# Performance work log

Hardware: AMD Instinct MI355X
Metric: run time of the kernel (lower is better)

## Reference

```python
import jax, jax.numpy as jnp
import numpy as np

HEADS = 8
DIM = 512
DIM_HEAD = DIM // 8          # 64
LANDMARKS = DIM // 2         # 256
PINV_ITERS = 6
KERNEL = 33                  # residual_conv_kernel default
SCALE = DIM_HEAD ** -0.5


def setup_inputs() -> dict:
    key = jax.random.key(0)
    k0, k1, k2, k3 = jax.random.split(key, 4)
    b, n = 2, 8192
    x = jax.random.normal(k0, (b, n, DIM), dtype=jnp.float32)
    inner = HEADS * DIM_HEAD
    w_qkv = jax.random.normal(k1, (DIM, 3 * inner), dtype=jnp.float32) * 0.02
    w_out = jax.random.normal(k2, (inner, DIM), dtype=jnp.float32) * 0.02
    b_out = jnp.zeros((DIM,), dtype=jnp.float32)
    # grouped depthwise-over-heads conv: (out_ch=H, in_ch/groups=1, kH=33, kW=1)
    w_conv = jax.random.normal(k3, (HEADS, 1, KERNEL, 1), dtype=jnp.float32) * 0.02
    return {"x": x, "w_qkv": w_qkv, "w_out": w_out, "b_out": b_out, "w_conv": w_conv}


def _moore_penrose_pinv(x, iters=PINV_ITERS):
    # x: [b, h, m, m]
    abs_x = jnp.abs(x)
    col = abs_x.sum(axis=-1).max()   # global max over col sums (matches torch.max)
    row = abs_x.sum(axis=-2).max()
    z = jnp.swapaxes(x, -1, -2) / (col * row)
    I = jnp.eye(x.shape[-1], dtype=x.dtype)
    for _ in range(iters):
        xz = x @ z
        z = 0.25 * z @ (13.0 * I - xz @ (15.0 * I - xz @ (7.0 * I - xz)))
    return z


def reference(x, w_qkv, w_out, b_out, w_conv):
    b, n, _ = x.shape
    m = LANDMARKS
    l = n // m  # n chosen divisible by m, so no left-padding branch

    qkv = x @ w_qkv                                   # [b, n, 3*inner]
    q, k, v = jnp.split(qkv, 3, axis=-1)
    to_heads = lambda t: t.reshape(b, n, HEADS, DIM_HEAD).transpose(0, 2, 1, 3)
    q = to_heads(q) * SCALE                           # [b, h, n, d]
    k = to_heads(k)
    v = to_heads(v)

    # landmarks: mean over consecutive groups of l tokens -> [b, h, m, d]
    q_l = q.reshape(b, HEADS, m, l, DIM_HEAD).mean(axis=3)
    k_l = k.reshape(b, HEADS, m, l, DIM_HEAD).mean(axis=3)

    sim1 = jnp.einsum('bhid,bhjd->bhij', q, k_l)      # [b, h, n, m]
    sim2 = jnp.einsum('bhid,bhjd->bhij', q_l, k_l)    # [b, h, m, m]
    sim3 = jnp.einsum('bhid,bhjd->bhij', q_l, k)      # [b, h, m, n]

    attn1 = jax.nn.softmax(sim1, axis=-1)
    attn2 = jax.nn.softmax(sim2, axis=-1)
    attn3 = jax.nn.softmax(sim3, axis=-1)

    attn2_inv = _moore_penrose_pinv(attn2)
    out = attn1 @ (attn2_inv @ (attn3 @ v))           # [b, h, n, d]

    # residual depthwise conv over the sequence dim, per head (groups = heads)
    pad = KERNEL // 2
    res = jax.lax.conv_general_dilated(
        v, w_conv, window_strides=(1, 1), padding=((pad, pad), (0, 0)),
        dimension_numbers=('NCHW', 'OIHW', 'NCHW'), feature_group_count=HEADS)
    out = out + res

    out = out.transpose(0, 2, 1, 3).reshape(b, n, HEADS * DIM_HEAD)
    out = out @ w_out + b_out                         # to_out (dropout = eval no-op)
    return x + out                                    # NyAttenLayer residual
```

## Files before the change

### kernel.cpp

```cpp
#include <hip/hip_runtime.h>
#include <hip/hip_bf16.h>

#define BH 16
#define NTOK 8192
#define NHEAD 8
#define DH 64
#define MLM 256
#define QSCALE 0.125f
#define LP 72
#define LOG2E 1.4426950408889634f

typedef unsigned short ushort_t;
using frag_ab = __attribute__((ext_vector_type(8))) short;
using frag_cd = __attribute__((ext_vector_type(4))) float;

__device__ __forceinline__ unsigned short f2bs(float f){
  __hip_bfloat16 h = __float2bfloat16(f);
  return *(unsigned short*)&h;
}
__device__ __forceinline__ float bs2f(unsigned short u){
  union { unsigned int i; float f; } cv; cv.i = ((unsigned int)u) << 16; return cv.f;
}

__device__ __forceinline__ void gl_lds16(const unsigned short* g, unsigned short* l){
  __builtin_amdgcn_global_load_lds((const __attribute__((address_space(1))) unsigned int*)(const void*)g,
                                   (__attribute__((address_space(3))) unsigned int*)(void*)l, 16, 0, 0);
}

__global__ __launch_bounds__(256) void k_splitw(const float* __restrict__ in, int K, int N,
                                                unsigned short* __restrict__ oh,
                                                unsigned short* __restrict__ ol, int swz){
  const int idx = blockIdx.x * 256 + threadIdx.x;
  const int n = idx / K, k = idx - n * K;
  const float v = in[(size_t)k * N + n];
  const unsigned short hi = f2bs(v);
  int kd = k;
  if (swz){
    const int q = (k >> 3) & 3;
    kd = (k & ~31) | (((q ^ (n & 3)) & 3) << 3) | (k & 7);
  }
  oh[(size_t)n * K + kd] = hi;
  ol[(size_t)n * K + kd] = f2bs(v - bs2f(hi));
}

__global__ __launch_bounds__(256) void k_splitx(const float* __restrict__ in,
                                                unsigned short* __restrict__ oh,
                                                unsigned short* __restrict__ ol){
  const size_t i4 = ((size_t)blockIdx.x * 256 + threadIdx.x) * 4;
  const int row = (int)(i4 >> 9);
  const int col = (int)(i4 & 511);
  const int q = (col >> 3) & 3;
  const int cd = (col & ~31) | (((q ^ (row & 3)) & 3) << 3) | (col & 7);
  const size_t o4 = ((size_t)row << 9) + cd;
  float4 v = *(const float4*)(in + i4);
  const unsigned short h0 = f2bs(v.x), h1 = f2bs(v.y), h2 = f2bs(v.z), h3 = f2bs(v.w);
  *(ushort4*)(oh + o4) = make_ushort4(h0, h1, h2, h3);
  *(ushort4*)(ol + o4) = make_ushort4(f2bs(v.x - bs2f(h0)), f2bs(v.y - bs2f(h1)),
                                      f2bs(v.z - bs2f(h2)), f2bs(v.w - bs2f(h3)));
}

__global__ __launch_bounds__(256) void k_mfma_qkv(const unsigned short* __restrict__ xh,
                                                  const unsigned short* __restrict__ xl,
                                                  const unsigned short* __restrict__ bth,
                                                  const unsigned short* __restrict__ btl,
                                                  float* __restrict__ q,
                                                  unsigned short* __restrict__ kSh,
                                                  unsigned short* __restrict__ kSl,
                                                  float* __restrict__ v){
  const int n0 = blockIdx.x * 128;
  const int m0 = blockIdx.y * 128;
  __shared__ unsigned short Ah[128*32], Al[128*32], Bh[128*32], Bl[128*32];
  const int tid = threadIdx.x;
  const int wave = tid >> 6, lane = tid & 63;
  const int wm = wave >> 1, wn = wave & 1;
  const int lr = lane & 15, quad = lane >> 4;
  const int cswz = ((quad ^ (lr & 3)) & 3) << 3;
  const unsigned short* gsrc = (wave == 0) ? xh : (wave == 1) ? xl : (wave == 2) ? bth : btl;
  unsigned short* lbase = (wave == 0) ? Ah : (wave == 1) ? Al : (wave == 2) ? Bh : Bl;
  const int R0 = (wave < 2) ? m0 : n0;
  const int lrow = lane >> 2, lslot = (lane & 3) << 3;
  frag_cd acc[4][4];
#pragma unroll
  for (int mt = 0; mt < 4; mt++)
#pragma unroll
    for (int nt = 0; nt < 4; nt++){
      frag_cd z = {0.f, 0.f, 0.f, 0.f};
      acc[mt][nt] = z;
    }
  for (int k0 = 0; k0 < 512; k0 += 32){
    __syncthreads();
#pragma unroll
    for (int u = 0; u < 8; u++){
      gl_lds16(gsrc + (size_t)(R0 + u*16 + lrow) * 512 + k0 + lslot, lbase + u * 512);
    }
    __syncthreads();
    frag_ab a_h[4], a_l[4], b_h[4], b_l[4];
#pragma unroll
    for (int t = 0; t < 4; t++){
      const int ar = (wm*64 + t*16 + lr) << 5;
      const int br = (wn*64 + t*16 + lr) << 5;
      a_h[t] = *(const frag_ab*)&Ah[ar + cswz];
      a_l[t] = *(const frag_ab*)&Al[ar + cswz];
      b_h[t] = *(const frag_ab*)&Bh[br + cswz];
      b_l[t] = *(const frag_ab*)&Bl[br + cswz];
    }
#pragma unroll
    for (int mt = 0; mt < 4; mt++)
#pragma unroll
      for (int nt = 0; nt < 4; nt++){
        acc[mt][nt] = __builtin_amdgcn_mfma_f32_16x16x32_bf16(a_l[mt], b_h[nt], acc[mt][nt], 0, 0, 0);
        acc[mt][nt] = __builtin_amdgcn_mfma_f32_16x16x32_bf16(a_h[mt], b_l[nt], acc[mt][nt], 0, 0, 0);
        acc[mt][nt] = __builtin_amdgcn_mfma_f32_16x16x32_bf16(a_h[mt], b_h[nt], acc[mt][nt], 0, 0, 0);
      }
  }
#pragma unroll
  for (int mt = 0; mt < 4; mt++)
#pragma unroll
    for (int nt = 0; nt < 4; nt++)
#pragma unroll
      for (int rg = 0; rg < 4; rg++){
        const int row = m0 + wm*64 + mt*16 + quad*4 + rg;
        const int col = n0 + wn*64 + nt*16 + lr;
        const int bb = row >> 13, i = row & 8191;
        const int which = col >> 9;
        const int cc = col & 511;
        const int h = cc >> 6, d = cc & 63;
        const size_t off = (((size_t)(bb * NHEAD + h)) * NTOK + i) * DH + d;
        const float val = acc[mt][nt][rg];
        if (which == 0)      q[off] = val * QSCALE;
        else if (which == 1){
          const unsigned short hi = f2bs(val);
          kSh[off] = hi; kSl[off] = f2bs(val - bs2f(hi));
        }
        else                 v[off] = val;
      }
}

__global__ __launch_bounds__(256) void k_mfma_final(const unsigned int* __restrict__ qpk,
                                                    const unsigned short* __restrict__ bth,
                                                    const unsigned short* __restrict__ btl,
                                                    const float* __restrict__ xin,
                                                    const float* __restrict__ bout,
                                                    float* __restrict__ outp){
  const int n0 = blockIdx.x * 128;
  const int m0 = blockIdx.y * 128;
  __shared__ unsigned short Ah[128][40], Al[128][40], Bh[128][40], Bl[128][40];
  const int tid = threadIdx.x;
  const int wave = tid >> 6, lane = tid & 63;
  const int wm = wave >> 1, wn = wave & 1;
  const int lr = lane & 15, quad = lane >> 4, koff = quad * 8;
  const int bb = m0 >> 13;
  frag_cd acc[4][4];
#pragma unroll
  for (int mt = 0; mt < 4; mt++)
#pragma unroll
    for (int nt = 0; nt < 4; nt++){
      frag_cd z = {0.f, 0.f, 0.f, 0.f};
      acc[mt][nt] = z;
    }
  for (int k0 = 0; k0 < 512; k0 += 32){
    const int h = k0 >> 6, dbase = k0 & 63;
    __syncthreads();
#pragma unroll
    for (int u = 0; u < 4; u++){
      const int f = tid + u * 256, row = f >> 3, c4 = (f & 7) << 2;
      const int i = (m0 + row) & 8191;
      uint4 pw = *(const uint4*)(qpk + (((size_t)(bb * NHEAD + h)) * NTOK + i) * DH + dbase + c4);
      *(ushort4*)&Ah[row][c4] = make_ushort4((unsigned short)pw.x, (unsigned short)pw.y,
                                             (unsigned short)pw.z, (unsigned short)pw.w);
      *(ushort4*)&Al[row][c4] = make_ushort4((unsigned short)(pw.x >> 16), (unsigned short)(pw.y >> 16),
                                             (unsigned short)(pw.z >> 16), (unsigned short)(pw.w >> 16));
    }
#pragma unroll
    for (int u = 0; u < 2; u++){
      const int f = tid + u * 256, row = f >> 2, ch = (f & 3) << 3;
      *(uint4*)&Bh[row][ch] = *(const uint4*)(bth + (size_t)(n0 + row) * 512 + k0 + ch);
      *(uint4*)&Bl[row][ch] = *(const uint4*)(btl + (size_t)(n0 + row) * 512 + k0 + ch);
    }
    __syncthreads();
    frag_ab a_h[4], a_l[4], b_h[4], b_l[4];
#pragma unroll
    for (int t = 0; t < 4; t++){
      a_h[t] = *(const frag_ab*)&Ah[wm*64 + t*16 + lr][koff];
      a_l[t] = *(const frag_ab*)&Al[wm*64 + t*16 + lr][koff];
      b_h[t] = *(const frag_ab*)&Bh[wn*64 + t*16 + lr][koff];
      b_l[t] = *(const frag_ab*)&Bl[wn*64 + t*16 + lr][koff];
    }
#pragma unroll
    for (int mt = 0; mt < 4; mt++)
#pragma unroll
      for (int nt = 0; nt < 4; nt++){
        acc[mt][nt] = __builtin_amdgcn_mfma_f32_16x16x32_bf16(a_l[mt], b_h[nt], acc[mt][nt], 0, 0, 0);
        acc[mt][nt] = __builtin_amdgcn_mfma_f32_16x16x32_bf16(a_h[mt], b_l[nt], acc[mt][nt], 0, 0, 0);
        acc[mt][nt] = __builtin_amdgcn_mfma_f32_16x16x32_bf16(a_h[mt], b_h[nt], acc[mt][nt], 0, 0, 0);
      }
  }
#pragma unroll
  for (int mt = 0; mt < 4; mt++)
#pragma unroll
    for (int nt = 0; nt < 4; nt++)
#pragma unroll
      for (int rg = 0; rg < 4; rg++){
        const int row = m0 + wm*64 + mt*16 + quad*4 + rg;
        const int col = n0 + wn*64 + nt*16 + lr;
        outp[(size_t)row * 512 + col] = acc[mt][nt][rg] + bout[col] + xin[(size_t)row * 512 + col];
      }
}

__global__ __launch_bounds__(64) void k_land2(const float* __restrict__ qf,
                                              const unsigned short* __restrict__ kSh,
                                              const unsigned short* __restrict__ kSl,
                                              float* __restrict__ qlf, float* __restrict__ klf,
                                              unsigned short* __restrict__ qlSh, unsigned short* __restrict__ qlSl,
                                              unsigned short* __restrict__ klSh, unsigned short* __restrict__ klSl){
  const int isK = blockIdx.y;
  float* dst = isK ? klf : qlf;
  unsigned short* dh = isK ? klSh : qlSh;
  unsigned short* dl = isK ? klSl : qlSl;
  const int bh = blockIdx.x >> 8;
  const int j  = blockIdx.x & 255;
  const int d  = threadIdx.x;
  const size_t base = ((size_t)bh * NTOK + (size_t)j * 32) * DH + d;
  float s = 0.f;
  if (!isK){
    const float* p = qf + base;
#pragma unroll
    for (int t = 0; t < 32; t++) s += p[t * DH];
  } else {
    const unsigned short* ph = kSh + base;
    const unsigned short* pl = kSl + base;
#pragma unroll
    for (int t = 0; t < 32; t++) s += bs2f(ph[t * DH]) + bs2f(pl[t * DH]);
  }
  const float val = s * (1.f / 32.f);
  const size_t oidx = ((size_t)bh * MLM + j) * DH + d;
  dst[oidx] = val;
  const unsigned short hi = f2bs(val);
  dh[oidx] = hi;
  dl[oidx] = f2bs(val - bs2f(hi));
}

__global__ __launch_bounds__(256) void k_vtrans(const float* __restrict__ vf,
                                                unsigned short* __restrict__ vTh,
                                                unsigned short* __restrict__ vTl){
  __shared__ float T[64][68];
  const int j0 = blockIdx.x * 64, bh = blockIdx.y;
  const int tid = threadIdx.x;
#pragma unroll
  for (int u = 0; u < 4; u++){
    const int f = tid + u * 256, row = f >> 4, c4 = (f & 15) << 2;
    *(float4*)&T[row][c4] = *(const float4*)(vf + ((size_t)bh * NTOK + j0 + row) * DH + c4);
  }
  __syncthreads();
#pragma unroll
  for (int u = 0; u < 4; u++){
    const int f = tid + u * 256, d = f >> 4, j4 = (f & 15) << 2;
    const float v0 = T[j4+0][d], v1 = T[j4+1][d], v2 = T[j4+2][d], v3 = T[j4+3][d];
    const unsigned short h0 = f2bs(v0), h1 = f2bs(v1), h2 = f2bs(v2), h3 = f2bs(v3);
    const size_t off = ((size_t)bh * DH + d) * NTOK + j0 + j4;
    *(ushort4*)(vTh + off) = make_ushort4(h0, h1, h2, h3);
    *(ushort4*)(vTl + off) = make_ushort4(f2bs(v0 - bs2f(h0)), f2bs(v1 - bs2f(h1)),
                                          f2bs(v2 - bs2f(h2)), f2bs(v3 - bs2f(h3)));
  }
}

__global__ __launch_bounds__(256) void k_sim2(const float* __restrict__ qlf,
                                              const float* __restrict__ klf,
                                              float* __restrict__ C){
  const int bh = blockIdx.z;
  const float* Ab = qlf + (size_t)bh * MLM * DH;
  const float* Bb = klf + (size_t)bh * MLM * DH;
  float* Cb = C + (size_t)bh * MLM * MLM;
  const int n0 = blockIdx.x * 64;
  const int m0 = blockIdx.y * 64;
  __shared__ float As[16][64];
  __shared__ float Bs[16][64];
  const int tid = threadIdx.x, ty = tid >> 4, tx = tid & 15;
  const int lm = tid >> 2, lk = (tid & 3) << 2;
  float acc[4][4] = {};
  for (int k0 = 0; k0 < 64; k0 += 16){
    float4 a4 = *(const float4*)(Ab + (size_t)(m0 + lm) * DH + k0 + lk);
    As[lk+0][lm] = a4.x; As[lk+1][lm] = a4.y; As[lk+2][lm] = a4.z; As[lk+3][lm] = a4.w;
    float4 b4 = *(const float4*)(Bb + (size_t)(n0 + lm) * DH + k0 + lk);
    Bs[lk+0][lm] = b4.x; Bs[lk+1][lm] = b4.y; Bs[lk+2][lm] = b4.z; Bs[lk+3][lm] = b4.w;
    __syncthreads();
#pragma unroll
    for (int kk = 0; kk < 16; kk++){
      float a[4], bv[4];
#pragma unroll
      for (int r = 0; r < 4; r++) a[r] = As[kk][ty*4 + r];
#pragma unroll
      for (int c = 0; c < 4; c++) bv[c] = Bs[kk][tx*4 + c];
#pragma unroll
      for (int r = 0; r < 4; r++)
#pragma unroll
        for (int c = 0; c < 4; c++) acc[r][c] += a[r] * bv[c];
    }
    __syncthreads();
  }
#pragma unroll
  for (int r = 0; r < 4; r++)
#pragma unroll
    for (int c = 0; c < 4; c++)
      Cb[(size_t)(m0 + ty*4 + r) * MLM + n0 + tx*4 + c] = acc[r][c];
}

__global__ __launch_bounds__(256) void k_softmax256(const float* __restrict__ in, float* __restrict__ outp){
  const int row = blockIdx.x;
  const int t = threadIdx.x;
  float v = in[(size_t)row * 256 + t];
  __shared__ float red[256];
  red[t] = v; __syncthreads();
  for (int o = 128; o > 0; o >>= 1){ if (t < o) red[t] = fmaxf(red[t], red[t+o]); __syncthreads(); }
  float mx = red[0]; __syncthreads();
  float e = exp2f((v - mx) * LOG2E);
  red[t] = e; __syncthreads();
  for (int o = 128; o > 0; o >>= 1){ if (t < o) red[t] += red[t+o]; __syncthreads(); }
  outp[(size_t)row * 256 + t] = e / red[0];
}

__global__ __launch_bounds__(256) void k_colrow(const float* __restrict__ a2, float* __restrict__ part){
  const int bh = blockIdx.x;
  const int t = threadIdx.x;
  const float* p = a2 + (size_t)bh * 65536;
  float cs = 0.f;
  for (int i = 0; i < 256; i++) cs += fabsf(p[(size_t)i * 256 + t]);
  __shared__ float r2[256];
  r2[t] = cs; __syncthreads();
  for (int o = 128; o > 0; o >>= 1){
    if (t < o) r2[t] = fmaxf(r2[t], r2[t+o]);
    __syncthreads();
  }
  if (t == 0) part[bh] = r2[0];
}

__global__ __launch_bounds__(256) void k_z0(const float* __restrict__ a2, const float* __restrict__ part,
                                            float* __restrict__ z,
                                            unsigned short* __restrict__ zTh,
                                            unsigned short* __restrict__ zTl){
  const int bh = blockIdx.x >> 8;
  const int i  = blockIdx.x & 255;
  const int j  = threadIdx.x;
  float m2 = 0.f;
#pragma unroll
  for (int t = 0; t < 16; t++) m2 = fmaxf(m2, part[t]);
  const float sc = 1.f / m2;
  const size_t ridx = ((size_t)bh * 256 + j) * 256 + i;
  const float val = a2[ridx] * sc;
  z[((size_t)bh * 256 + i) * 256 + j] = val;
  const unsigned short hi = f2bs(val);
  zTh[ridx] = hi;
  zTl[ridx] = f2bs(val - bs2f(hi));
}

__global__ __launch_bounds__(256) void k_gemm256m(const float* __restrict__ A,
                                                  const unsigned short* __restrict__ BTh,
                                                  const unsigned short* __restrict__ BTl,
                                                  const float* __restrict__ D,
                                                  float* __restrict__ C,
                                                  unsigned short* __restrict__ CTh,
                                                  unsigned short* __restrict__ CTl,
                                                  float c0, float s0, int wC){
  __shared__ unsigned short Ah[32][40], Al[32][40], Bh[64][40], Bl[64][40];
  __shared__ float Ct[64][33];
  const int bh = blockIdx.y, tile = blockIdx.x;
  const int m0 = (tile >> 2) * 32, n0 = (tile & 3) * 64;
  const size_t bo = (size_t)bh * 65536;
  const int tid = threadIdx.x;
  const int wave = tid >> 6, lane = tid & 63;
  const int wm = wave >> 1, wn = wave & 1;
  const int lr = lane & 15, quad = lane >> 4, koff = quad * 8;
  const int ar = tid >> 3, ac = (tid & 7) << 2;
  const int br = tid >> 2, bc = (tid & 3) << 3;
  frag_cd acc[2];
  { frag_cd z = {0.f,0.f,0.f,0.f}; acc[0] = z; acc[1] = z; }
  float4 ra  = *(const float4*)(A + bo + (size_t)(m0 + ar) * 256 + ac);
  uint4  rbh = *(const uint4*)(BTh + bo + (size_t)(n0 + br) * 256 + bc);
  uint4  rbl = *(const uint4*)(BTl + bo + (size_t)(n0 + br) * 256 + bc);
  for (int k0 = 0; k0 < 256; k0 += 32){
    __syncthreads();
    {
      const unsigned short h0=f2bs(ra.x),h1=f2bs(ra.y),h2=f2bs(ra.z),h3=f2bs(ra.w);
      *(ushort4*)&Ah[ar][ac] = make_ushort4(h0,h1,h2,h3);
      *(ushort4*)&Al[ar][ac] = make_ushort4(f2bs(ra.x-bs2f(h0)), f2bs(ra.y-bs2f(h1)),
                                            f2bs(ra.z-bs2f(h2)), f2bs(ra.w-bs2f(h3)));
      *(uint4*)&Bh[br][bc] = rbh;
      *(uint4*)&Bl[br][bc] = rbl;
    }
    __syncthreads();
    if (k0 < 224){
      ra  = *(const float4*)(A + bo + (size_t)(m0 + ar) * 256 + k0 + 32 + ac);
      rbh = *(const uint4*)(BTh + bo + (size_t)(n0 + br) * 256 + k0 + 32 + bc);
      rbl = *(const uint4*)(BTl + bo + (size_t)(n0 + br) * 256 + k0 + 32 + bc);
    }
    frag_ab a_h = *(const frag_ab*)&Ah[wm*16 + lr][koff];
    frag_ab a_l = *(const frag_ab*)&Al[wm*16 + lr][koff];
#pragma unroll
    for (int b = 0; b < 2; b++){
      frag_ab b_h = *(const frag_ab*)&Bh[wn*32 + b*16 + lr][koff];
      frag_ab b_l = *(const frag_ab*)&Bl[wn*32 + b*16 + lr][koff];
      acc[b] = __builtin_amdgcn_mfma_f32_16x16x32_bf16(a_l, b_l, acc[b], 0, 0, 0);
      acc[b] = __builtin_amdgcn_mfma_f32_16x16x32_bf16(a_l, b_h, acc[b], 0, 0, 0);
      acc[b] = __builtin_amdgcn_mfma_f32_16x16x32_bf16(a_h, b_l, acc[b], 0, 0, 0);
      acc[b] = __builtin_amdgcn_mfma_f32_16x16x32_bf16(a_h, b_h, acc[b], 0, 0, 0);
    }
  }
  const bool useD = (c0 != 0.f);
#pragma unroll
  for (int b = 0; b < 2; b++)
#pragma unroll
    for (int rg = 0; rg < 4; rg++){
      const int row = m0 + wm*16 + quad*4 + rg;
      const int col = n0 + wn*32 + b*16 + lr;
      const size_t idx = bo + (size_t)row * 256 + col;
      const float dv = useD ? D[idx] : 0.f;
      const float val = s0 * (c0 * dv - acc[b][rg]);
      if (wC) C[idx] = val;
      Ct[col - n0][row - m0] = val;
    }
  __syncthreads();
  {
    const int cr = tid >> 2, sg = (tid & 3) << 3;
    unsigned int ph[4], pl[4];
#pragma unroll
    for (int j = 0; j < 4; j++){
      const float v0 = Ct[cr][sg + 2*j], v1 = Ct[cr][sg + 2*j + 1];
      const unsigned short h0 = f2bs(v0), h1 = f2bs(v1);
      ph[j] = (unsigned int)h0 | ((unsigned int)h1 << 16);
      pl[j] = (unsigned int)f2bs(v0 - bs2f(h0)) | ((unsigned int)f2bs(v1 - bs2f(h1)) << 16);
    }
    const size_t tb = bo + (size_t)(n0 + cr) * 256 + m0 + sg;
    *(uint4*)(CTh + tb) = make_uint4(ph[0], ph[1], ph[2], ph[3]);
    *(uint4*)(CTl + tb) = make_uint4(pl[0], pl[1], pl[2], pl[3]);
  }
}

__global__ __launch_bounds__(256) void k_flash(const unsigned short* __restrict__ qlSh,
                                               const unsigned short* __restrict__ qlSl,
                                               const unsigned short* __restrict__ kSh,
                                               const unsigned short* __restrict__ kSl,
                                               const unsigned short* __restrict__ vTh,
                                               const unsigned short* __restrict__ vTl,
                                               float* __restrict__ pbuf){
  extern __shared__ __align__(16) unsigned short sm[];
  unsigned short* Kh  = sm;
  unsigned short* Kl  = sm + 1*64*LP;
  unsigned short* Wth = sm + 2*64*LP;
  unsigned short* Wtl = sm + 3*64*LP;
  const int kc = blockIdx.x, mt = blockIdx.y, bh = blockIdx.z;
  const int m0 = mt * 64, kbeg = kc * 512;
  const int tid = threadIdx.x;
  const int wave = tid >> 6, lane = tid & 63;
  const int lr = lane & 15, quad = lane >> 4;
  const size_t qbase = (size_t)bh * MLM * DH;
  const size_t kb  = (size_t)bh * NTOK * DH;
  const size_t vtb = (size_t)bh * DH * NTOK;
#pragma unroll
  for (int u = 0; u < 4; u++){
    const int f = tid + u * 256, row = f >> 4, c4 = (f & 15) << 2;
    *(ushort4*)&Kh[row*LP + c4] = *(const ushort4*)(qlSh + qbase + (size_t)(m0 + row) * DH + c4);
    *(ushort4*)&Kl[row*LP + c4] = *(const ushort4*)(qlSl + qbase + (size_t)(m0 + row) * DH + c4);
  }
  __syncthreads();
  frag_ab qa_h[2], qa_l[2];
#pragma unroll
  for (int ks = 0; ks < 2; ks++){
    const int ao = (wave*16 + lr)*LP + ks*32 + quad*8;
    qa_h[ks] = *(const frag_ab*)&Kh[ao];
    qa_l[ks] = *(const frag_ab*)&Kl[ao];
  }
  float m_run[4], l_run[4];
  frag_cd o[4];
#pragma unroll
  for (int r = 0; r < 4; r++){ m_run[r] = -1e30f; l_run[r] = 0.f; }
#pragma unroll
  for (int nt = 0; nt < 4; nt++){ frag_cd z = {0.f,0.f,0.f,0.f}; o[nt] = z; }

  for (int ch = 0; ch < 8; ch++){
    const int kr0 = kbeg + ch * 64;
    __syncthreads();
#pragma unroll
    for (int u = 0; u < 4; u++){
      const int f = tid + u * 256, row = f >> 4, c4 = (f & 15) << 2;
      *(ushort4*)&Kh[row*LP + c4]  = *(const ushort4*)(kSh + kb + (size_t)(kr0 + row) * DH + c4);
      *(ushort4*)&Kl[row*LP + c4]  = *(const ushort4*)(kSl + kb + (size_t)(kr0 + row) * DH + c4);
      *(ushort4*)&Wth[row*LP + c4] = *(const ushort4*)(vTh + vtb + (size_t)row * NTOK + kr0 + c4);
      *(ushort4*)&Wtl[row*LP + c4] = *(const ushort4*)(vTl + vtb + (size_t)row * NTOK + kr0 + c4);
    }
    __syncthreads();
    frag_cd s[4];
#pragma unroll
    for (int nt = 0; nt < 4; nt++){ frag_cd z = {0.f,0.f,0.f,0.f}; s[nt] = z; }
#pragma unroll
    for (int ks = 0; ks < 2; ks++){
#pragma unroll
      for (int nt = 0; nt < 4; nt++){
        const int bo = (nt*16 + lr)*LP + ks*32 + quad*8;
        frag_ab b_h = *(const frag_ab*)&Kh[bo];
        frag_ab b_l = *(const frag_ab*)&Kl[bo];
        s[nt] = __builtin_amdgcn_mfma_f32_16x16x32_bf16(qa_l[ks], b_h, s[nt], 0, 0, 0);
        s[nt] = __builtin_amdgcn_mfma_f32_16x16x32_bf16(qa_h[ks], b_l, s[nt], 0, 0, 0);
        s[nt] = __builtin_amdgcn_mfma_f32_16x16x32_bf16(qa_h[ks], b_h, s[nt], 0, 0, 0);
      }
    }
    __syncthreads();
#pragma unroll
    for (int rg = 0; rg < 4; rg++){
      float mx = fmaxf(fmaxf(s[0][rg], s[1][rg]), fmaxf(s[2][rg], s[3][rg]));
#pragma unroll
      for (int o2 = 8; o2 >= 1; o2 >>= 1) mx = fmaxf(mx, __shfl_xor(mx, o2));
      const float mnew = fmaxf(m_run[rg], mx);
      float e0 = exp2f((s[0][rg] - mnew) * LOG2E), e1 = exp2f((s[1][rg] - mnew) * LOG2E);
      float e2 = exp2f((s[2][rg] - mnew) * LOG2E), e3 = exp2f((s[3][rg] - mnew) * LOG2E);
      float psum = e0 + e1 + e2 + e3;
#pragma unroll
      for (int o2 = 8; o2 >= 1; o2 >>= 1) psum += __shfl_xor(psum, o2);
      const float alpha = exp2f((m_run[rg] - mnew) * LOG2E);
      l_run[rg] = l_run[rg] * alpha + psum;
      m_run[rg] = mnew;
#pragma unroll
      for (int nt = 0; nt < 4; nt++) o[nt][rg] *= alpha;
      const int prow = (wave*16 + quad*4 + rg) * LP;
      float ee[4] = {e0, e1, e2, e3};
#pragma unroll
      for (int nt = 0; nt < 4; nt++){
        const unsigned short hh = f2bs(ee[nt]);
        Kh[prow + nt*16 + lr] = hh;
        Kl[prow + nt*16 + lr] = f2bs(ee[nt] - bs2f(hh));
      }
    }
#pragma unroll
    for (int ks = 0; ks < 2; ks++){
      const int ao = (wave*16 + lr)*LP + ks*32 + quad*8;
      frag_ab p_h = *(const frag_ab*)&Kh[ao];
      frag_ab p_l = *(const frag_ab*)&Kl[ao];
#pragma unroll
      for (int nt = 0; nt < 4; nt++){
        const int bo = (nt*16 + lr)*LP + ks*32 + quad*8;
        frag_ab b_h = *(const frag_ab*)&Wth[bo];
        frag_ab b_l = *(const frag_ab*)&Wtl[bo];
        o[nt] = __builtin_amdgcn_mfma_f32_16x16x32_bf16(p_l, b_h, o[nt], 0, 0, 0);
        o[nt] = __builtin_amdgcn_mfma_f32_16x16x32_bf16(p_h, b_l, o[nt], 0, 0, 0);
        o[nt] = __builtin_amdgcn_mfma_f32_16x16x32_bf16(p_h, b_h, o[nt], 0, 0, 0);
      }
    }
  }
  float* pb = pbuf + (((size_t)bh * 16 + kc) * 256 + m0) * 68;
#pragma unroll
  for (int rg = 0; rg < 4; rg++){
    const int row = wave*16 + quad*4 + rg;
#pragma unroll
    for (int nt = 0; nt < 4; nt++)
      pb[(size_t)row * 68 + nt*16 + lr] = o[nt][rg];
    if (lr == 0){
      pb[(size_t)row * 68 + 64] = m_run[rg];
      pb[(size_t)row * 68 + 65] = l_run[rg];
    }
  }
}

__global__ __launch_bounds__(256) void k_comb(const float* __restrict__ pbuf, float* __restrict__ av){
  const int wv = threadIdx.x >> 6, lane = threadIdx.x & 63;
  const int id = blockIdx.x * 4 + wv;
  const int bh = id >> 8, row = id & 255;
  const float* base = pbuf + ((size_t)bh * 16 * 256 + row) * 68;
  float M = -1e30f;
#pragma unroll
  for (int k = 0; k < 16; k++) M = fmaxf(M, base[(size_t)k * 256 * 68 + 64]);
  float L = 0.f, o = 0.f;
#pragma unroll
  for (int k = 0; k < 16; k++){
    const float* p = base + (size_t)k * 256 * 68;
    float w = exp2f((p[64] - M) * LOG2E);
    L += p[65] * w;
    o += p[lane] * w;
  }
  av[((size_t)bh * MLM + row) * DH + lane] = o / L;
}

__global__ __launch_bounds__(256) void k_w2(const float* __restrict__ Z, const float* __restrict__ AV,
                                            float* __restrict__ W2,
                                            unsigned short* __restrict__ w2Th,
                                            unsigned short* __restrict__ w2Tl){
  const int bh = blockIdx.y, mt = blockIdx.x;
  const float* Zb = Z + (size_t)bh * 65536;
  const float* Vb = AV + (size_t)bh * MLM * DH;
  float* Wb = W2 + (size_t)bh * MLM * DH;
  const int m0 = mt * 64;
  __shared__ float As[16][64];
  __shared__ float Bs[16][64];
  const int tid = threadIdx.x, ty = tid >> 4, tx = tid & 15;
  const int lm = tid >> 2, lk = (tid & 3) << 2;
  const int lk2 = tid >> 4, ln = (tid & 15) << 2;
  float acc[4][4] = {};
  for (int k0 = 0; k0 < 256; k0 += 16){
    float4 a4 = *(const float4*)(Zb + (size_t)(m0 + lm) * 256 + k0 + lk);
    As[lk+0][lm] = a4.x; As[lk+1][lm] = a4.y; As[lk+2][lm] = a4.z; As[lk+3][lm] = a4.w;
    float4 b4 = *(const float4*)(Vb + (size_t)(k0 + lk2) * DH + ln);
    *(float4*)&Bs[lk2][ln] = b4;
    __syncthreads();
#pragma unroll
    for (int kk = 0; kk < 16; kk++){
      float a[4], bv[4];
#pragma unroll
      for (int r = 0; r < 4; r++) a[r] = As[kk][ty*4 + r];
#pragma unroll
      for (int c = 0; c < 4; c++) bv[c] = Bs[kk][tx*4 + c];
#pragma unroll
      for (int r = 0; r < 4; r++)
#pragma unroll
        for (int c = 0; c < 4; c++) acc[r][c] += a[r] * bv[c];
    }
    __syncthreads();
  }
#pragma unroll
  for (int r = 0; r < 4; r++)
#pragma unroll
    for (int c = 0; c < 4; c++){
      const float val = acc[r][c];
      Wb[(size_t)(m0 + ty*4 + r) * DH + tx*4 + c] = val;
      const unsigned short hi = f2bs(val);
      const size_t tidx = ((size_t)bh * DH + tx*4 + c) * MLM + m0 + ty*4 + r;
      w2Th[tidx] = hi;
      w2Tl[tidx] = f2bs(val - bs2f(hi));
    }
}

__global__ __launch_bounds__(512) void k_attn1(float* __restrict__ qoh,
                                               const unsigned short* __restrict__ klSh,
                                               const unsigned short* __restrict__ klSl,
                                               const float* __restrict__ vf,
                                               const unsigned short* __restrict__ w2Th,
                                               const unsigned short* __restrict__ w2Tl,
                                               const float* __restrict__ wconv){
  extern __shared__ __align__(16) unsigned short sm[];
  unsigned short* Kh  = sm;
  unsigned short* Kl  = sm + 1*64*LP;
  unsigned short* Wth = sm + 2*64*LP;
  unsigned short* Wtl = sm + 3*64*LP;
  unsigned short* Ph  = sm + 4*64*LP;
  unsigned short* Pl  = sm + 6*64*LP;
  float (*Vs)[68] = (float (*)[68])sm;
  float (*St)[68] = (float (*)[68])sm;
  __shared__ float wcs[33];
  const int it = blockIdx.x, bh = blockIdx.y, h = bh & 7;
  const int i0 = it * 128;
  float* qb = qoh + (size_t)bh * NTOK * DH;
  const int tid = threadIdx.x;
  const int wave = tid >> 6, lane = tid & 63;
  const int lr = lane & 15, quad = lane >> 4;
  if (tid < 33) wcs[tid] = wconv[h*33 + tid];
  frag_ab qa_h[2], qa_l[2];
#pragma unroll
  for (int ks = 0; ks < 2; ks++){
    const float* qsrc = qb + (size_t)(i0 + wave*16 + lr) * DH + ks*32 + quad*8;
    float4 a0 = *(const float4*)qsrc;
    float4 a1 = *(const float4*)(qsrc + 4);
    float vv[8] = {a0.x, a0.y, a0.z, a0.w, a1.x, a1.y, a1.z, a1.w};
    frag_ab fh, fl;
#pragma unroll
    for (int j = 0; j < 8; j++){
      const unsigned short hb = f2bs(vv[j]);
      fh[j] = (short)hb;
      fl[j] = (short)f2bs(vv[j] - bs2f(hb));
    }
    qa_h[ks] = fh; qa_l[ks] = fl;
  }
  float m_run[4], l_run[4];
  frag_cd o[4];
#pragma unroll
  for (int r = 0; r < 4; r++){ m_run[r] = -1e30f; l_run[r] = 0.f; }
#pragma unroll
  for (int nt = 0; nt < 4; nt++){ frag_cd z = {0.f,0.f,0.f,0.f}; o[nt] = z; }
  const size_t klbase = (size_t)bh * MLM * DH;
  const size_t wtbase = (size_t)bh * DH * MLM;

  for (int jc = 0; jc < 4; jc++){
    const int j0 = jc * 64;
    __syncthreads();
#pragma unroll
    for (int u = 0; u < 2; u++){
      const int f = tid + u * 512, row = f >> 4, c4 = (f & 15) << 2;
      *(ushort4*)&Kh[row*LP + c4]  = *(const ushort4*)(klSh + klbase + (size_t)(j0 + row) * DH + c4);
      *(ushort4*)&Kl[row*LP + c4]  = *(const ushort4*)(klSl + klbase + (size_t)(j0 + row) * DH + c4);
      *(ushort4*)&Wth[row*LP + c4] = *(const ushort4*)(w2Th + wtbase + (size_t)row * MLM + j0 + c4);
      *(ushort4*)&Wtl[row*LP + c4] = *(const ushort4*)(w2Tl + wtbase + (size_t)row * MLM + j0 + c4);
    }
    __syncthreads();
    frag_cd s[4];
#pragma unroll
    for (int nt = 0; nt < 4; nt++){ frag_cd z = {0.f,0.f,0.f,0.f}; s[nt] = z; }
#pragma unroll
    for (int ks = 0; ks < 2; ks++){
#pragma unroll
      for (int nt = 0; nt < 4; nt++){
        const int bo = (nt*16 + lr)*LP + ks*32 + quad*8;
        frag_ab b_h = *(const frag_ab*)&Kh[bo];
        frag_ab b_l = *(const frag_ab*)&Kl[bo];
        s[nt] = __builtin_amdgcn_mfma_f32_16x16x32_bf16(qa_l[ks], b_h, s[nt], 0, 0, 0);
        s[nt] = __builtin_amdgcn_mfma_f32_16x16x32_bf16(qa_h[ks], b_l, s[nt], 0, 0, 0);
        s[nt] = __builtin_amdgcn_mfma_f32_16x16x32_bf16(qa_h[ks], b_h, s[nt], 0, 0, 0);
      }
    }
#pragma unroll
    for (int rg = 0; rg < 4; rg++){
      float mx = fmaxf(fmaxf(s[0][rg], s[1][rg]), fmaxf(s[2][rg], s[3][rg]));
#pragma unroll
      for (int o2 = 8; o2 >= 1; o2 >>= 1) mx = fmaxf(mx, __shfl_xor(mx, o2));
      const float mnew = fmaxf(m_run[rg], mx);
      float e0 = exp2f((s[0][rg] - mnew) * LOG2E), e1 = exp2f((s[1][rg] - mnew) * LOG2E);
      float e2 = exp2f((s[2][rg] - mnew) * LOG2E), e3 = exp2f((s[3][rg] - mnew) * LOG2E);
      float psum = e0 + e1 + e2 + e3;
#pragma unroll
      for (int o2 = 8; o2 >= 1; o2 >>= 1) psum += __shfl_xor(psum, o2);
      const float alpha = exp2f((m_run[rg] - mnew) * LOG2E);
      l_run[rg] = l_run[rg] * alpha + psum;
      m_run[rg] = mnew;
#pragma unroll
      for (int nt = 0; nt < 4; nt++) o[nt][rg] *= alpha;
      const int prow = (wave*16 + quad*4 + rg) * LP;
      float ee[4] = {e0, e1, e2, e3};
#pragma unroll
      for (int nt = 0; nt < 4; nt++){
        const unsigned short hh = f2bs(ee[nt]);
        Ph[prow + nt*16 + lr] = hh;
        Pl[prow + nt*16 + lr] = f2bs(ee[nt] - bs2f(hh));
      }
    }
#pragma unroll
    for (int ks = 0; ks < 2; ks++){
      const int ao = (wave*16 + lr)*LP + ks*32 + quad*8;
      frag_ab p_h = *(const frag_ab*)&Ph[ao];
      frag_ab p_l = *(const frag_ab*)&Pl[ao];
#pragma unroll
      for (int nt = 0; nt < 4; nt++){
        const int bo = (nt*16 + lr)*LP + ks*32 + quad*8;
        frag_ab b_h = *(const frag_ab*)&Wth[bo];
        frag_ab b_l = *(const frag_ab*)&Wtl[bo];
        o[nt] = __builtin_amdgcn_mfma_f32_16x16x32_bf16(p_l, b_h, o[nt], 0, 0, 0);
        o[nt] = __builtin_amdgcn_mfma_f32_16x16x32_bf16(p_h, b_l, o[nt], 0, 0, 0);
        o[nt] = __builtin_amdgcn_mfma_f32_16x16x32_bf16(p_h, b_h, o[nt], 0, 0, 0);
      }
    }
  }
#pragma unroll
  for (int rg = 0; rg < 4; rg++){
    const float inv = 1.f / l_run[rg];
#pragma unroll
    for (int nt = 0; nt < 4; nt++) o[nt][rg] *= inv;
  }
  __syncthreads();
#pragma unroll
  for (int u = 0; u < 5; u++){
    const int f = tid + u * 512, row = f >> 4, c4 = (f & 15) << 2;
    const int g = i0 - 16 + row;
    float4 vv = make_float4(0.f, 0.f, 0.f, 0.f);
    if (g >= 0 && g < NTOK) vv = *(const float4*)(vf + ((size_t)bh * NTOK + g) * DH + c4);
    *(float4*)&Vs[row][c4] = vv;
  }
  __syncthreads();
  const int rbase = wave*16 + quad*4;
#pragma unroll
  for (int nt = 0; nt < 4; nt++){
    const int col = nt*16 + lr;
#pragma unroll
    for (int s5 = 0; s5 < 36; s5++){
      const float v = Vs[rbase + s5][col];
#pragma unroll
      for (int rg = 0; rg < 4; rg++){
        const int t = s5 - rg;
        if (t >= 0 && t <= 32) o[nt][rg] += wcs[t] * v;
      }
    }
  }
  __syncthreads();
#pragma unroll
  for (int nt = 0; nt < 4; nt++)
#pragma unroll
    for (int rg = 0; rg < 4; rg++){
      const float val = o[nt][rg];
      const unsigned short hi = f2bs(val);
      const unsigned short lo = f2bs(val - bs2f(hi));
      St[rbase + rg][nt*16 + lr] = __uint_as_float((unsigned int)hi | ((unsigned int)lo << 16));
    }
  __syncthreads();
#pragma unroll
  for (int u = 0; u < 4; u++){
    const int f = tid + u * 512, row = f >> 4, c4 = (f & 15) << 2;
    *(float4*)(qb + (size_t)(i0 + row) * DH + c4) = *(const float4*)&St[row][c4];
  }
}

extern "C" void kernel_launch(void* const* d_in, const int* in_sizes, int n_in,
                              void* d_out, int out_size, void* d_ws, size_t ws_size,
                              hipStream_t stream){
  (void)in_sizes; (void)n_in; (void)out_size; (void)ws_size;
  const float* x     = (const float*)d_in[0];
  const float* wqkv  = (const float*)d_in[1];
  const float* wout  = (const float*)d_in[2];
  const float* bout  = (const float*)d_in[3];
  const float* wconv = (const float*)d_in[4];
  float* outp = (float*)d_out;

  char* base = (char*)d_ws;
  auto alloc = [&](size_t bytes)->char*{
    char* p = base; base += (bytes + 255) & ~(size_t)255; return p;
  };
  const size_t QS = (size_t)BH * NTOK * DH;
  const size_t LS = (size_t)BH * MLM * DH;
  const size_t MM = (size_t)BH * MLM * MLM;

  float* qf   = (float*)alloc(QS * 4);
  float* vf   = (float*)alloc(QS * 4);
  unsigned short* kSh = (unsigned short*)alloc(QS * 2);
  unsigned short* kSl = (unsigned short*)alloc(QS * 2);
  float* qlf  = (float*)alloc(LS * 4);
  float* klf  = (float*)alloc(LS * 4);
  float* a2   = (float*)alloc(MM * 4);
  float* zb   = (float*)alloc(MM * 4);
  float* z2   = (float*)alloc(MM * 4);
  float* xz   = (float*)alloc(MM * 4);
  float* t2   = (float*)alloc(MM * 4);
  float* t4   = (float*)alloc(MM * 4);
  float* part = (float*)alloc(64 * 4);
  char* un = alloc(10 * MM * 2);
  unsigned short* pl0 = (unsigned short*)un;
  unsigned short* zbTh = pl0 + 0*MM; unsigned short* zbTl = pl0 + 1*MM;
  unsigned short* z2Th = pl0 + 2*MM; unsigned short* z2Tl = pl0 + 3*MM;
  unsigned short* xzTh = pl0 + 4*MM; unsigned short* xzTl = pl0 + 5*MM;
  unsigned short* t2Th = pl0 + 6*MM; unsigned short* t2Tl = pl0 + 7*MM;
  unsigned short* t4Th = pl0 + 8*MM; unsigned short* t4Tl = pl0 + 9*MM;
  float* pbuf = (float*)un;
  float* av   = (float*)alloc(LS * 4);
  float* w2   = (float*)alloc(LS * 4);
  unsigned short* wqTh = (unsigned short*)alloc((size_t)1536 * 512 * 2);
  unsigned short* wqTl = (unsigned short*)alloc((size_t)1536 * 512 * 2);
  unsigned short* woTh = (unsigned short*)alloc((size_t)512 * 512 * 2);
  unsigned short* woTl = (unsigned short*)alloc((size_t)512 * 512 * 2);
  unsigned short* qlSh = (unsigned short*)alloc(LS * 2);
  unsigned short* qlSl = (unsigned short*)alloc(LS * 2);
  unsigned short* klSh = (unsigned short*)alloc(LS * 2);
  unsigned short* klSl = (unsigned short*)alloc(LS * 2);
  unsigned short* w2Th = (unsigned short*)alloc(LS * 2);
  unsigned short* w2Tl = (unsigned short*)alloc(LS * 2);
  unsigned short* vTh  = (unsigned short*)alloc(QS * 2);
  unsigned short* vTl  = (unsigned short*)alloc(QS * 2);
  unsigned short* xh = vTh;
  unsigned short* xl = vTl;

  k_splitw<<<1536 * 512 / 256, 256, 0, stream>>>(wqkv, 512, 1536, wqTh, wqTl, 1);
  k_splitw<<<512 * 512 / 256, 256, 0, stream>>>(wout, 512, 512, woTh, woTl, 0);
  k_splitx<<<8192, 256, 0, stream>>>(x, xh, xl);
  k_mfma_qkv<<<dim3(12, 128), 256, 0, stream>>>(xh, xl, wqTh, wqTl, qf, kSh, kSl, vf);
  k_vtrans<<<dim3(NTOK / 64, BH), 256, 0, stream>>>(vf, vTh, vTl);
  k_land2<<<dim3(BH * MLM, 2), 64, 0, stream>>>(qf, kSh, kSl, qlf, klf, qlSh, qlSl, klSh, klSl);
  k_sim2<<<dim3(4, 4, BH), 256, 0, stream>>>(qlf, klf, xz);
  k_softmax256<<<BH * MLM, 256, 0, stream>>>(xz, a2);
  k_colrow<<<BH, 256, 0, stream>>>(a2, part);
  k_z0<<<BH * MLM, 256, 0, stream>>>(a2, part, zb, zbTh, zbTl);
  {
    float* zc = zb;  unsigned short* zcTh = zbTh; unsigned short* zcTl = zbTl;
    float* zn = z2;  unsigned short* znTh = z2Th; unsigned short* znTl = z2Tl;
    for (int it = 0; it < 6; ++it){
      k_gemm256m<<<dim3(32, BH), 256, 0, stream>>>(a2, zcTh, zcTl, a2, xz, xzTh, xzTl, 0.f, -1.f, 1);
      k_gemm256m<<<dim3(32, BH), 256, 0, stream>>>(xz, xzTh, xzTl, xz, t2, t2Th, t2Tl, 7.f, 1.f, 0);
      k_gemm256m<<<dim3(32, BH), 256, 0, stream>>>(xz, t2Th, t2Tl, xz, t4, t4Th, t4Tl, 15.f, 1.f, 0);
      k_gemm256m<<<dim3(32, BH), 256, 0, stream>>>(zc, t4Th, t4Tl, zc, zn, znTh, znTl, 13.f, 0.25f, 1);
      float* tf = zc; zc = zn; zn = tf;
      unsigned short* th = zcTh; zcTh = znTh; znTh = th;
      unsigned short* tl = zcTl; zcTl = znTl; znTl = tl;
    }
  }
  const size_t FLASH_LDS = (size_t)4 * 64 * LP * 2;
  const size_t ATTN1_LDS = (size_t)8 * 64 * LP * 2;
  k_flash<<<dim3(16, 4, BH), 256, FLASH_LDS, stream>>>(qlSh, qlSl, kSh, kSl, vTh, vTl, pbuf);
  k_comb<<<BH * MLM / 4, 256, 0, stream>>>(pbuf, av);
  k_w2<<<dim3(4, BH), 256, 0, stream>>>(zb, av, w2, w2Th, w2Tl);
  k_attn1<<<dim3(64, BH), 512, ATTN1_LDS, stream>>>(qf, klSh, klSl, vf, w2Th, w2Tl, wconv);
  k_mfma_final<<<dim3(4, 128), 256, 0, stream>>>((const unsigned int*)qf, woTh, woTl, x, bout, outp);
}
```

Before: 695.9 us.

## Double-buffer QKV GEMM LDS, prefetch out-proj A tile, drop lo*lo MFMA

The QKV projection GEMM now uses two LDS buffers. The next K-slice is loaded asynchronously into the alternate buffer while MFMAs run on the current one, which cuts one barrier per iteration. The output-projection GEMM prefetches the next packed Q/attention tile into registers before the compute step, so global latency is hidden behind the MFMAs. The pinv GEMM drops the low×low bf16 split-product term, reducing its MFMA work by a quarter at a small accuracy cost in the Newton–Schulz iterations. Double buffering doubles the QKV kernel's LDS use (64KB), which may reduce occupancy.

```diff
diff --git a/kernel.cpp b/kernel.cpp
--- a/kernel.cpp
+++ b/kernel.cpp
@@ -69,16 +69,16 @@
                                                   float* __restrict__ v){
   const int n0 = blockIdx.x * 128;
   const int m0 = blockIdx.y * 128;
-  __shared__ unsigned short Ah[128*32], Al[128*32], Bh[128*32], Bl[128*32];
+  __shared__ unsigned short SB[2][4 * 128 * 32];
   const int tid = threadIdx.x;
   const int wave = tid >> 6, lane = tid & 63;
   const int wm = wave >> 1, wn = wave & 1;
   const int lr = lane & 15, quad = lane >> 4;
   const int cswz = ((quad ^ (lr & 3)) & 3) << 3;
   const unsigned short* gsrc = (wave == 0) ? xh : (wave == 1) ? xl : (wave == 2) ? bth : btl;
-  unsigned short* lbase = (wave == 0) ? Ah : (wave == 1) ? Al : (wave == 2) ? Bh : Bl;
   const int R0 = (wave < 2) ? m0 : n0;
   const int lrow = lane >> 2, lslot = (lane & 3) << 3;
+  const int pbase = wave * 4096;
   frag_cd acc[4][4];
 #pragma unroll
   for (int mt = 0; mt < 4; mt++)
@@ -87,13 +87,22 @@
       frag_cd z = {0.f, 0.f, 0.f, 0.f};
       acc[mt][nt] = z;
     }
+#pragma unroll
+  for (int u = 0; u < 8; u++)
+    gl_lds16(gsrc + (size_t)(R0 + u*16 + lrow) * 512 + lslot, &SB[0][pbase] + u * 512);
+  __syncthreads();
+  int cur = 0;
   for (int k0 = 0; k0 < 512; k0 += 32){
-    __syncthreads();
-#pragma unroll
-    for (int u = 0; u < 8; u++){
-      gl_lds16(gsrc + (size_t)(R0 + u*16 + lrow) * 512 + k0 + lslot, lbase + u * 512);
-    }
-    __syncthreads();
+    if (k0 + 32 < 512){
+#pragma unroll
+      for (int u = 0; u < 8; u++)
+        gl_lds16(gsrc + (size_t)(R0 + u*16 + lrow) * 512 + k0 + 32 + lslot,
+                 &SB[cur ^ 1][pbase] + u * 512);
+    }
+    const unsigned short* Ah = &SB[cur][0];
+    const unsigned short* Al = &SB[cur][4096];
+    const unsigned short* Bh = &SB[cur][8192];
+    const unsigned short* Bl = &SB[cur][12288];
     frag_ab a_h[4], a_l[4], b_h[4], b_l[4];
 #pragma unroll
     for (int t = 0; t < 4; t++){
@@ -112,6 +121,8 @@
         acc[mt][nt] = __builtin_amdgcn_mfma_f32_16x16x32_bf16(a_h[mt], b_l[nt], acc[mt][nt], 0, 0, 0);
         acc[mt][nt] = __builtin_amdgcn_mfma_f32_16x16x32_bf16(a_h[mt], b_h[nt], acc[mt][nt], 0, 0, 0);
       }
+    __syncthreads();
+    cur ^= 1;
   }
 #pragma unroll
   for (int mt = 0; mt < 4; mt++)
@@ -158,26 +169,41 @@
       frag_cd z = {0.f, 0.f, 0.f, 0.f};
       acc[mt][nt] = z;
     }
+  const int arow = tid >> 3, ac4 = (tid & 7) << 2;
+  const int brow = tid >> 2, bch = (tid & 3) << 3;
+  uint4 pw[4];
+#pragma unroll
+  for (int u = 0; u < 4; u++){
+    const int row = arow + u * 32;
+    const int i = (m0 + row) & 8191;
+    pw[u] = *(const uint4*)(qpk + (((size_t)(bb * NHEAD + 0)) * NTOK + i) * DH + 0 + ac4);
+  }
   for (int k0 = 0; k0 < 512; k0 += 32){
-    const int h = k0 >> 6, dbase = k0 & 63;
     __syncthreads();
 #pragma unroll
     for (int u = 0; u < 4; u++){
-      const int f = tid + u * 256, row = f >> 3, c4 = (f & 7) << 2;
-      const int i = (m0 + row) & 8191;
-      uint4 pw = *(const uint4*)(qpk + (((size_t)(bb * NHEAD + h)) * NTOK + i) * DH + dbase + c4);
-      *(ushort4*)&Ah[row][c4] = make_ushort4((unsigned short)pw.x, (unsigned short)pw.y,
-                                             (unsigned short)pw.z, (unsigned short)pw.w);
-      *(ushort4*)&Al[row][c4] = make_ushort4((unsigned short)(pw.x >> 16), (unsigned short)(pw.y >> 16),
-                                             (unsigned short)(pw.z >> 16), (unsigned short)(pw.w >> 16));
+      const int row = arow + u * 32;
+      *(ushort4*)&Ah[row][ac4] = make_ushort4((unsigned short)pw[u].x, (unsigned short)pw[u].y,
+                                              (unsigned short)pw[u].z, (unsigned short)pw[u].w);
+      *(ushort4*)&Al[row][ac4] = make_ushort4((unsigned short)(pw[u].x >> 16), (unsigned short)(pw[u].y >> 16),
+                                              (unsigned short)(pw[u].z >> 16), (unsigned short)(pw[u].w >> 16));
     }
 #pragma unroll
     for (int u = 0; u < 2; u++){
-      const int f = tid + u * 256, row = f >> 2, ch = (f & 3) << 3;
-      *(uint4*)&Bh[row][ch] = *(const uint4*)(bth + (size_t)(n0 + row) * 512 + k0 + ch);
-      *(uint4*)&Bl[row][ch] = *(const uint4*)(btl + (size_t)(n0 + row) * 512 + k0 + ch);
-    }
-    __syncthreads();
+      const int row = brow + u * 64;
+      *(uint4*)&Bh[row][bch] = *(const uint4*)(bth + (size_t)(n0 + row) * 512 + k0 + bch);
+      *(uint4*)&Bl[row][bch] = *(const uint4*)(btl + (size_t)(n0 + row) * 512 + k0 + bch);
+    }
+    __syncthreads();
+    if (k0 + 32 < 512){
+      const int hn = (k0 + 32) >> 6, dbn = (k0 + 32) & 63;
+#pragma unroll
+      for (int u = 0; u < 4; u++){
+        const int row = arow + u * 32;
+        const int i = (m0 + row) & 8191;
+        pw[u] = *(const uint4*)(qpk + (((size_t)(bb * NHEAD + hn)) * NTOK + i) * DH + dbn + ac4);
+      }
+    }
     frag_ab a_h[4], a_l[4], b_h[4], b_l[4];
 #pragma unroll
     for (int t = 0; t < 4; t++){
@@ -399,7 +425,6 @@
     for (int b = 0; b < 2; b++){
       frag_ab b_h = *(const frag_ab*)&Bh[wn*32 + b*16 + lr][koff];
       frag_ab b_l = *(const frag_ab*)&Bl[wn*32 + b*16 + lr][koff];
-      acc[b] = __builtin_amdgcn_mfma_f32_16x16x32_bf16(a_l, b_l, acc[b], 0, 0, 0);
       acc[b] = __builtin_amdgcn_mfma_f32_16x16x32_bf16(a_l, b_h, acc[b], 0, 0, 0);
       acc[b] = __builtin_amdgcn_mfma_f32_16x16x32_bf16(a_h, b_l, acc[b], 0, 0, 0);
       acc[b] = __builtin_amdgcn_mfma_f32_16x16x32_bf16(a_h, b_h, acc[b], 0, 0, 0);
```

After: 680.7 us (median of 2 runs). -2.2%, faster.
